# Kernel optimization log

Hardware: AMD Instinct MI355X
Metric: run time of the kernel (lower is better)

The kernel has to match this reference:

```python
import jax, jax.numpy as jnp
from jax import lax
import numpy as np

B, N_VARS, M_CLAUSES, K_DIM = 1024, 64, 256, 12
MAX_ITER = 12


def setup_inputs() -> dict:
    key = jax.random.key(0)
    k1, k2, k3, k4 = jax.random.split(key, 4)
    z = jax.random.uniform(k1, (B, N_VARS), dtype=jnp.float32)          # input probabilities
    S = jax.random.normal(k2, (M_CLAUSES, N_VARS + 1), dtype=jnp.float32) * 0.2  # learnable clause matrix (col 0 = truth var)
    w = jax.random.uniform(k3, (M_CLAUSES,), dtype=jnp.float32)          # learnable clause weights
    r = jax.random.normal(k4, (B, N_VARS, K_DIM), dtype=jnp.float32)     # random init directions
    return {"z": z, "S": S, "w": w, "r": r, "max_iter": MAX_ITER}


def _mixing(z, S, w, r, max_iter):
    Bsz, n = z.shape
    m, N = S.shape  # N = n + 1 (truth variable is column 0)
    k = r.shape[-1]
    eps = jnp.float32(1e-8)

    # truth direction v_T = e_0
    vT = jnp.zeros((k,), dtype=z.dtype).at[0].set(1.0)

    # random unit directions orthogonal to v_T (zero out component along e_0)
    r_perp = r.at[..., 0].set(0.0)
    r_perp = r_perp / jnp.maximum(jnp.linalg.norm(r_perp, axis=-1, keepdims=True), eps)

    # SATNet init: v_i = -cos(pi z_i) v_T + sin(pi z_i) r_perp_i
    ang = jnp.pi * z
    Vvars = -jnp.cos(ang)[..., None] * vT + jnp.sin(ang)[..., None] * r_perp  # [B,n,k]
    V = jnp.concatenate([jnp.broadcast_to(vT, (Bsz, 1, k)), Vvars], axis=1)   # [B,N,k]

    Sw = S * w[:, None]                       # weighted clause matrix [m,N]
    W = jnp.einsum('mn,bnk->bmk', Sw, V)      # running product Sw @ V, [B,m,k]
    snrm = jnp.sum(Sw * Sw, axis=0)           # ||s_i||^2 per variable, [N]

    def coord_step(carry, i):
        V, W = carry
        s_i = Sw[:, i]                         # [m]
        v_old = V[:, i, :]                     # [B,k]
        g = jnp.einsum('bmk,m->bk', W, s_i) - snrm[i] * v_old
        v_new = -g / jnp.maximum(jnp.linalg.norm(g, axis=-1, keepdims=True), eps)
        W = W + (v_new - v_old)[:, None, :] * s_i[None, :, None]  # rank-1 update
        V = V.at[:, i, :].set(v_new)
        return (V, W), None

    def sweep(carry, _):
        carry, _ = lax.scan(coord_step, carry, jnp.arange(1, N))  # coordinate descent over variables
        return carry, None

    (V, _), _ = lax.scan(sweep, (V, W), None, length=max_iter)

    # output probabilities: z_i = arccos(-v_i . v_T) / pi
    cos = jnp.clip(-V[:, 1:, 0], -1.0 + 1e-6, 1.0 - 1e-6)
    return jnp.arccos(cos) / jnp.pi


def reference(z, S, w, r, max_iter):
    return _mixing(z, S, w, r, max_iter)
```

## Files before the change

### kernel.cpp

```cpp
#include <hip/hip_runtime.h>
#include <math.h>

#define BATCH 1024
#define NV    64
#define MC    256
#define KD    12
#define PI_F  3.14159265358979323846f

#define C0OFF  4096
#define DGAOFF 4160
#define DGBOFF 4224
#define CBUF   4288

typedef float f2  __attribute__((ext_vector_type(2)));
typedef float v4f __attribute__((ext_vector_type(4)));
typedef __attribute__((address_space(3))) float lds_f;

__device__ __forceinline__ f2 bc2(float x) { f2 y; y.x = x; y.y = x; return y; }
__device__ __forceinline__ f2 fma2(f2 a, f2 b, f2 c) {
  return __builtin_elementwise_fma(a, b, c);
}

template <int CTRL>
__device__ __forceinline__ float dpp_addf(float x) {
  int y = __builtin_amdgcn_update_dpp(0, __float_as_int(x), CTRL, 0xF, 0xF, true);
  return x + __int_as_float(y);
}
__device__ __forceinline__ float readlane63(float x) {
  return __int_as_float(__builtin_amdgcn_readlane(__float_as_int(x), 63));
}
__device__ __forceinline__ float rlane(float x, int i) {
  return __int_as_float(__builtin_amdgcn_readlane(__float_as_int(x), i));
}

template <int IMM>
__device__ __forceinline__ void dsr(v4f& d, unsigned base) {
  asm volatile("ds_read_b128 %0, %1 offset:%2" : "=v"(d) : "v"(base), "i"(IMM));
}

__global__ void compute_C_kernel(const float* __restrict__ S,
                                 const float* __restrict__ w,
                                 float* __restrict__ Cg, int nsplit) {
  const int q = blockIdx.x;
  const int mc = blockIdx.y;
  const int j = threadIdx.x;
  if (j > NV) return;
  const int v = (q + 1) % 64 + 1;
  const int mlen = MC / nsplit;
  const int m0 = mc * mlen;
  float a0 = 0.f, a1 = 0.f, a2 = 0.f, a3 = 0.f;
  for (int m = m0; m < m0 + mlen; m += 4) {
    const float w0 = w[m], w1 = w[m + 1], w2 = w[m + 2], w3 = w[m + 3];
    a0 = fmaf(S[(m + 0) * (NV + 1) + v] * w0 * w0, S[(m + 0) * (NV + 1) + j], a0);
    a1 = fmaf(S[(m + 1) * (NV + 1) + v] * w1 * w1, S[(m + 1) * (NV + 1) + j], a1);
    a2 = fmaf(S[(m + 2) * (NV + 1) + v] * w2 * w2, S[(m + 2) * (NV + 1) + j], a2);
    a3 = fmaf(S[(m + 3) * (NV + 1) + v] * w3 * w3, S[(m + 3) * (NV + 1) + j], a3);
  }
  const float acc = (a0 + a1) + (a2 + a3);
  float* buf = Cg + mc * CBUF;
  const int p1 = (v == 1) ? 64 : (v - 1);
  const int p2 = (v == 1) ? 63 : (v == 2) ? 64 : (v - 2);
  if (j == 0) buf[C0OFF + q] = acc;
  if (j == p1) buf[DGAOFF + (v - 1)] = acc;
  if (j == p2) buf[DGBOFF + (v - 1)] = acc;
  if (j > 0) {
    const int j0 = j - 1;
    const float st = (j == v || j == p1 || j == p2) ? 0.f : acc;
    buf[q * 64 + (j0 & 7) * 8 + (j0 >> 3)] = st;
  }
}

__global__ __launch_bounds__(256, 1) void mixing_kernel(
    const float* __restrict__ z, const float* __restrict__ r,
    const float* __restrict__ Cg, const int* __restrict__ max_iter_p,
    float* __restrict__ out, int nsplit) {
  __shared__ __align__(16) float Ls[CBUF];

  const int t = threadIdx.x;
  const int l = t & 63;
  const int jgx = (l & 3) | ((l >> 1) & 4);
  const int kl = ((l >> 2) & 1) | ((l >> 3) & 6);
  const int b = blockIdx.x * 4 + (t >> 6);
  const int max_iter = max_iter_p[0];

  {
    const float4* src = (const float4*)Cg;
    float4* dst = (float4*)Ls;
    for (int idx = t; idx < CBUF / 4; idx += 256) {
      float4 a = src[idx];
      for (int u = 1; u < nsplit; ++u) {
        const float4 p = src[u * (CBUF / 4) + idx];
        a.x += p.x; a.y += p.y; a.z += p.z; a.w += p.w;
      }
      dst[idx] = a;
    }
  }

  const float my_e0 = (kl == 0) ? 1.f : 0.f;

  f2 Vv[8];
  #pragma unroll
  for (int m = 0; m < 8; ++m) {
    const int j0 = jgx + 8 * m;
    const float zv = z[b * NV + j0];
    f2 rp = bc2(0.f);
    if (kl < 6) rp = *(const f2*)&r[(b * NV + j0) * KD + 2 * kl];
    if (kl == 0) rp.x = 0.f;
    float ssp = fmaf(rp.x, rp.x, rp.y * rp.y);
    ssp += __shfl_xor(ssp, 4, 64);
    ssp += __shfl_xor(ssp, 16, 64);
    ssp += __shfl_xor(ssp, 32, 64);
    const float inv = 1.f / fmaxf(sqrtf(ssp), 1e-8f);
    const float sn = __builtin_amdgcn_sinf(0.5f * zv);
    const float cs = __builtin_amdgcn_cosf(0.5f * zv);
    const float si = sn * inv;
    Vv[m].x = (kl == 0) ? -cs : si * rp.x;
    Vv[m].y = si * rp.y;
  }

  __syncthreads();

  const float t0v = Ls[C0OFF + l];
  const float t1v = Ls[DGAOFF + l];
  const float t2v = Ls[DGBOFF + l];

  f2 P, vp1, vp2;

  {
    const v4f cA = *(const v4f*)&Ls[63 * 64 + jgx * 8];
    const v4f cB = *(const v4f*)&Ls[63 * 64 + jgx * 8 + 4];
    f2 q = bc2(cA.x) * Vv[0];
    q = fma2(bc2(cA.y), Vv[1], q);
    q = fma2(bc2(cA.z), Vv[2], q);
    q = fma2(bc2(cA.w), Vv[3], q);
    q = fma2(bc2(cB.x), Vv[4], q);
    q = fma2(bc2(cB.y), Vv[5], q);
    q = fma2(bc2(cB.z), Vv[6], q);
    q = fma2(bc2(cB.w), Vv[7], q);
    q.x = dpp_addf<0xB1>(q.x);  q.y = dpp_addf<0xB1>(q.y);
    q.x = dpp_addf<0x4E>(q.x);  q.y = dpp_addf<0x4E>(q.y);
    q.x = dpp_addf<0x128>(q.x); q.y = dpp_addf<0x128>(q.y);
    q.x = fmaf(my_e0, Ls[C0OFF + 63], q.x);
    P = q;
    vp1.x = __shfl(Vv[7].x, (l & 0x34) | 0x0B, 64);
    vp1.y = __shfl(Vv[7].y, (l & 0x34) | 0x0B, 64);
    vp2.x = __shfl(Vv[7].x, (l & 0x34) | 0x0A, 64);
    vp2.y = __shfl(Vv[7].y, (l & 0x34) | 0x0A, 64);
  }

  const unsigned lbase = (unsigned)(unsigned long long)(lds_f*)&Ls[jgx * 8];

  v4f Rb[8][2];

#define PFROW(R) \
  dsr<((((R) & 63) * 256) + 0)>(Rb[(R) & 7][0], lbase); \
  dsr<((((R) & 63) * 256) + 16)>(Rb[(R) & 7][1], lbase);

#define WAITR4(I) \
  asm volatile("s_waitcnt lgkmcnt(4)" \
               : "+v"(Rb[(I) & 7][0]), "+v"(Rb[(I) & 7][1]), \
                 "+v"(Rb[((I) + 1) & 7][0]), "+v"(Rb[((I) + 1) & 7][1]), \
                 "+v"(Rb[((I) + 2) & 7][0]), "+v"(Rb[((I) + 2) & 7][1]), \
                 "+v"(Rb[((I) + 3) & 7][0]), "+v"(Rb[((I) + 3) & 7][1]));

#define STEPC(I) { \
  constexpr int i_ = (I); \
  constexpr int sl_ = i_ & 7; \
  constexpr int j0w_ = (i_ + 63) & 63; \
  constexpr int m_ = j0w_ >> 3; \
  constexpr int jgo_ = j0w_ & 7; \
  const float da_ = rlane(t1v, i_); \
  const float db_ = rlane(t2v, i_); \
  const float c0_ = rlane(t0v, i_); \
   \
  f2 g_ = fma2(bc2(da_), vp1, fma2(bc2(db_), vp2, P)); \
  float t_ = fmaf(g_.x, g_.x, g_.y * g_.y); \
  const v4f ceA = Rb[sl_][0], ceB = Rb[sl_][1]; \
   \
  f2 qa_ = bc2(ceA.x) * Vv[0]; \
  f2 qb_ = bc2(ceB.x) * Vv[4]; \
  qa_ = fma2(bc2(ceA.y), Vv[1], qa_); \
  qb_ = fma2(bc2(ceB.y), Vv[5], qb_); \
  t_ = dpp_addf<0x124>(t_);             \
  qa_ = fma2(bc2(ceA.z), Vv[2], qa_); \
  qb_ = fma2(bc2(ceB.z), Vv[6], qb_); \
  t_ = dpp_addf<0x142>(t_);             \
  qa_ = fma2(bc2(ceA.w), Vv[3], qa_); \
  qb_ = fma2(bc2(ceB.w), Vv[7], qb_); \
  t_ = dpp_addf<0x143>(t_);             \
  f2 q_ = qa_ + qb_; \
  const float n2_ = readlane63(t_); \
  const float inv_ = __builtin_amdgcn_rsqf(fmaxf(n2_, 1e-16f)); \
  q_.x = dpp_addf<0xB1>(q_.x);  q_.y = dpp_addf<0xB1>(q_.y); \
  const f2 vn_ = g_ * bc2(-inv_); \
  q_.x = dpp_addf<0x4E>(q_.x);  q_.y = dpp_addf<0x4E>(q_.y); \
  q_.x = dpp_addf<0x128>(q_.x); q_.y = dpp_addf<0x128>(q_.y); \
  q_.x = fmaf(my_e0, c0_, q_.x); \
   \
  Vv[m_].x = (jgx == jgo_) ? vp1.x : Vv[m_].x; \
  Vv[m_].y = (jgx == jgo_) ? vp1.y : Vv[m_].y; \
   \
  vp2 = vp1; vp1 = vn_; P = q_; \
}

#define QUAD(I) { WAITR4(I) \
                  STEPC(I) STEPC((I) + 1) STEPC((I) + 2) STEPC((I) + 3) \
                  PFROW((I) + 6) PFROW((I) + 7) PFROW((I) + 8) PFROW((I) + 9) }

#define Q16(N) QUAD(N) QUAD((N) + 4) QUAD((N) + 8) QUAD((N) + 12)

  asm volatile("s_waitcnt lgkmcnt(0)" ::: "memory");
  PFROW(0) PFROW(1) PFROW(2) PFROW(3) PFROW(4) PFROW(5)

  #pragma unroll 1
  for (int it = 0; it < max_iter; ++it) {
    Q16(0) Q16(16) Q16(32) Q16(48)
  }

  Vv[7].x = (jgx == 7) ? vp1.x : Vv[7].x;
  Vv[7].y = (jgx == 7) ? vp1.y : Vv[7].y;

  asm volatile("s_waitcnt lgkmcnt(0)" ::: "memory");
  __syncthreads();
  {
    float* Lw = Ls + (t >> 6) * 64;
    if (kl == 0) {
      #pragma unroll
      for (int m = 0; m < 8; ++m) Lw[jgx + 8 * m] = Vv[m].x;
    }
    __builtin_amdgcn_s_waitcnt(0);
    float cv = -Lw[l];
    cv = fminf(fmaxf(cv, -1.f + 1e-6f), 1.f - 1e-6f);
    out[b * NV + l] = acosf(cv) * (1.f / PI_F);
  }
}

extern "C" void kernel_launch(void* const* d_in, const int* in_sizes, int n_in,
                              void* d_out, int out_size, void* d_ws, size_t ws_size,
                              hipStream_t stream) {
  const float* z = (const float*)d_in[0];
  const float* S = (const float*)d_in[1];
  const float* w = (const float*)d_in[2];
  const float* r = (const float*)d_in[3];
  const int* max_iter = (const int*)d_in[4];
  float* Cg = (float*)d_ws;

  const int nsplit = (ws_size >= (size_t)8 * CBUF * 4) ? 8
                   : (ws_size >= (size_t)4 * CBUF * 4) ? 4 : 1;
  compute_C_kernel<<<dim3(NV, nsplit), 128, 0, stream>>>(S, w, Cg, nsplit);
  mixing_kernel<<<BATCH / 4, 256, 0, stream>>>(z, r, Cg, max_iter,
                                               (float*)d_out, nsplit);
}
```

Measured before the change: 137.0 us.

## Prefetch per-step scalar coefficients from LDS and restructure prefetch pipeline into pairs

The per-step coefficients (c0, two diagonal couplings) now sit packed as float4 in an LDS table and are fetched with ds_read_b128 inside the software pipeline. This replaces three v_readlane operations per coordinate step, which serialise on the scalar path. The prefetch schedule changes from quads with a 6-row lookahead to pairs with a 3-4 step lookahead and lgkmcnt(3) waits. The fmax clamp before rsq is also replaced by adding a tiny epsilon inside the norm accumulation, which changes behaviour slightly for near-zero gradients.

Result: no change. 138.2 us (+0.9%).

```diff
diff --git a/kernel.cpp b/kernel.cpp
--- a/kernel.cpp
+++ b/kernel.cpp
@@ -7,10 +7,8 @@
 #define KD    12
 #define PI_F  3.14159265358979323846f
 
-#define C0OFF  4096
-#define DGAOFF 4160
-#define DGBOFF 4224
-#define CBUF   4288
+#define TBOFF  4096
+#define CBUF   4352
 
 typedef float f2  __attribute__((ext_vector_type(2)));
 typedef float v4f __attribute__((ext_vector_type(4)));
@@ -28,9 +26,6 @@
 }
 __device__ __forceinline__ float readlane63(float x) {
   return __int_as_float(__builtin_amdgcn_readlane(__float_as_int(x), 63));
-}
-__device__ __forceinline__ float rlane(float x, int i) {
-  return __int_as_float(__builtin_amdgcn_readlane(__float_as_int(x), i));
 }
 
 template <int IMM>
@@ -60,9 +55,12 @@
   float* buf = Cg + mc * CBUF;
   const int p1 = (v == 1) ? 64 : (v - 1);
   const int p2 = (v == 1) ? 63 : (v == 2) ? 64 : (v - 2);
-  if (j == 0) buf[C0OFF + q] = acc;
-  if (j == p1) buf[DGAOFF + (v - 1)] = acc;
-  if (j == p2) buf[DGBOFF + (v - 1)] = acc;
+  if (j == 0) {
+    buf[TBOFF + q * 4 + 0] = acc;
+    buf[TBOFF + q * 4 + 3] = 0.f;
+  }
+  if (j == p1) buf[TBOFF + (v - 1) * 4 + 1] = acc;
+  if (j == p2) buf[TBOFF + (v - 1) * 4 + 2] = acc;
   if (j > 0) {
     const int j0 = j - 1;
     const float st = (j == v || j == p1 || j == p2) ? 0.f : acc;
@@ -120,10 +118,6 @@
 
   __syncthreads();
 
-  const float t0v = Ls[C0OFF + l];
-  const float t1v = Ls[DGAOFF + l];
-  const float t2v = Ls[DGBOFF + l];
-
   f2 P, vp1, vp2;
 
   {
@@ -140,7 +134,7 @@
     q.x = dpp_addf<0xB1>(q.x);  q.y = dpp_addf<0xB1>(q.y);
     q.x = dpp_addf<0x4E>(q.x);  q.y = dpp_addf<0x4E>(q.y);
     q.x = dpp_addf<0x128>(q.x); q.y = dpp_addf<0x128>(q.y);
-    q.x = fmaf(my_e0, Ls[C0OFF + 63], q.x);
+    q.x = fmaf(my_e0, Ls[TBOFF + 63 * 4 + 0], q.x);
     P = q;
     vp1.x = __shfl(Vv[7].x, (l & 0x34) | 0x0B, 64);
     vp1.y = __shfl(Vv[7].y, (l & 0x34) | 0x0B, 64);
@@ -149,19 +143,23 @@
   }
 
   const unsigned lbase = (unsigned)(unsigned long long)(lds_f*)&Ls[jgx * 8];
+  const unsigned tbase = (unsigned)(unsigned long long)(lds_f*)&Ls[0];
 
   v4f Rb[8][2];
+  v4f Tb[8];
 
 #define PFROW(R) \
   dsr<((((R) & 63) * 256) + 0)>(Rb[(R) & 7][0], lbase); \
   dsr<((((R) & 63) * 256) + 16)>(Rb[(R) & 7][1], lbase);
-
-#define WAITR4(I) \
-  asm volatile("s_waitcnt lgkmcnt(4)" \
-               : "+v"(Rb[(I) & 7][0]), "+v"(Rb[(I) & 7][1]), \
+#define PFTAB(R) \
+  dsr<(TBOFF * 4 + (((R) & 63) * 16))>(Tb[(R) & 7], tbase);
+#define PFSTEP(R) PFROW(R) PFTAB(R)
+
+#define WAITP(I) \
+  asm volatile("s_waitcnt lgkmcnt(3)" \
+               : "+v"(Rb[(I) & 7][0]), "+v"(Rb[(I) & 7][1]), "+v"(Tb[(I) & 7]), \
                  "+v"(Rb[((I) + 1) & 7][0]), "+v"(Rb[((I) + 1) & 7][1]), \
-                 "+v"(Rb[((I) + 2) & 7][0]), "+v"(Rb[((I) + 2) & 7][1]), \
-                 "+v"(Rb[((I) + 3) & 7][0]), "+v"(Rb[((I) + 3) & 7][1]));
+                 "+v"(Tb[((I) + 1) & 7]));
 
 #define STEPC(I) { \
   constexpr int i_ = (I); \
@@ -169,12 +167,13 @@
   constexpr int j0w_ = (i_ + 63) & 63; \
   constexpr int m_ = j0w_ >> 3; \
   constexpr int jgo_ = j0w_ & 7; \
-  const float da_ = rlane(t1v, i_); \
-  const float db_ = rlane(t2v, i_); \
-  const float c0_ = rlane(t0v, i_); \
+  const v4f tt_ = Tb[sl_]; \
+  const float c0_ = tt_.x, da_ = tt_.y, db_ = tt_.z; \
    \
   f2 g_ = fma2(bc2(da_), vp1, fma2(bc2(db_), vp2, P)); \
-  float t_ = fmaf(g_.x, g_.x, g_.y * g_.y); \
+   \
+   \
+  float t_ = fmaf(g_.x, g_.x, fmaf(g_.y, g_.y, 2e-17f)); \
   const v4f ceA = Rb[sl_][0], ceB = Rb[sl_][1]; \
    \
   f2 qa_ = bc2(ceA.x) * Vv[0]; \
@@ -190,7 +189,7 @@
   t_ = dpp_addf<0x143>(t_);             \
   f2 q_ = qa_ + qb_; \
   const float n2_ = readlane63(t_); \
-  const float inv_ = __builtin_amdgcn_rsqf(fmaxf(n2_, 1e-16f)); \
+  const float inv_ = __builtin_amdgcn_rsqf(n2_); \
   q_.x = dpp_addf<0xB1>(q_.x);  q_.y = dpp_addf<0xB1>(q_.y); \
   const f2 vn_ = g_ * bc2(-inv_); \
   q_.x = dpp_addf<0x4E>(q_.x);  q_.y = dpp_addf<0x4E>(q_.y); \
@@ -203,18 +202,18 @@
   vp2 = vp1; vp1 = vn_; P = q_; \
 }
 
-#define QUAD(I) { WAITR4(I) \
-                  STEPC(I) STEPC((I) + 1) STEPC((I) + 2) STEPC((I) + 3) \
-                  PFROW((I) + 6) PFROW((I) + 7) PFROW((I) + 8) PFROW((I) + 9) }
-
-#define Q16(N) QUAD(N) QUAD((N) + 4) QUAD((N) + 8) QUAD((N) + 12)
+#define PAIR2(I) { WAITP(I) PFSTEP((I) + 3) PFSTEP((I) + 4) \
+                   STEPC(I) STEPC((I) + 1) }
+
+#define PR8(N)  PAIR2(N) PAIR2((N) + 2) PAIR2((N) + 4) PAIR2((N) + 6)
+#define PR32(N) PR8((N) + 0) PR8((N) + 8) PR8((N) + 16) PR8((N) + 24)
 
   asm volatile("s_waitcnt lgkmcnt(0)" ::: "memory");
-  PFROW(0) PFROW(1) PFROW(2) PFROW(3) PFROW(4) PFROW(5)
+  PFSTEP(0) PFSTEP(1) PFSTEP(2)
 
   #pragma unroll 1
   for (int it = 0; it < max_iter; ++it) {
-    Q16(0) Q16(16) Q16(32) Q16(48)
+    PR32(0) PR32(32)
   }
 
   Vv[7].x = (jgx == 7) ? vp1.x : Vv[7].x;
```
